# Performance work log

Hardware: AMD Instinct MI355X
Metric: run time of the kernel (lower is better)

Reference implementation:

```python
import jax, jax.numpy as jnp
import numpy as np

HID = 2048
HEADS = 16
HD = HID // HEADS  # 128
EPS = 1e-6


def setup_inputs() -> dict:
    key = jax.random.key(0)
    ks = jax.random.split(key, 9)
    s = 1.0 / np.sqrt(HID)
    return {
        "hidden_states": jax.random.normal(ks[0], (4, 4096, HID), jnp.float32),
        "q_w": jax.random.normal(ks[1], (HID, HID), jnp.float32) * s,
        "q_b": jnp.zeros((HID,), jnp.float32),
        "k_w": jax.random.normal(ks[2], (HID, HID), jnp.float32) * s,
        "k_b": jnp.zeros((HID,), jnp.float32),
        "v_w": jax.random.normal(ks[3], (HID, HID), jnp.float32) * s,
        "v_b": jnp.zeros((HID,), jnp.float32),
        "o_w": jax.random.normal(ks[4], (HID, HID), jnp.float32) * s,
        "o_b": jnp.zeros((HID,), jnp.float32),
    }


def _heads(x, b, s):
    # [B,S,HID] -> [B,H,S,Dh]
    return x.reshape(b, s, HEADS, HD).transpose(0, 2, 1, 3)


def reference(hidden_states, q_w, q_b, k_w, k_b, v_w, v_b, o_w, o_b):
    b, s, _ = hidden_states.shape
    # torch Linear: y = x @ W.T + b
    q = _heads(hidden_states @ q_w.T + q_b, b, s)
    k = _heads(hidden_states @ k_w.T + k_b, b, s)
    v = _heads(hidden_states @ v_w.T + v_b, b, s)
    # kernel feature map: elu(x) + 1
    qp = jax.nn.elu(q) + 1.0
    kp = jax.nn.elu(k) + 1.0
    # KV outer-product reduction over sequence: [B,H,Dh,Dh]
    kv = jnp.einsum('bhsd,bhse->bhde', kp, v)
    # normalizer z = q' @ sum_s k'  -> [B,H,S,1]
    z = jnp.einsum('bhsd,bhd->bhs', qp, kp.sum(axis=2))[..., None]
    attn = jnp.einsum('bhsd,bhde->bhse', qp, kv) / (z + EPS)
    out = attn.transpose(0, 2, 1, 3).reshape(b, s, HID)
    return out @ o_w.T + o_b
```

## Files before the change

### kernel.cpp

```cpp
#include <hip/hip_runtime.h>
#include <hip/hip_bf16.h>

#define HIDC 2048
#define NHEADS 16
#define HDIM 128
#define NB 4
#define NS 4096
#define NROWS (NB*NS)
#define QSTR 6144
#define EPSV 1e-6f

typedef __attribute__((ext_vector_type(8))) short s16x8;
typedef __attribute__((ext_vector_type(4))) float f32x4;
typedef __attribute__((ext_vector_type(8))) unsigned short u16x8;

static __device__ __forceinline__ unsigned short f2b(float f) {
  unsigned int u = __float_as_uint(f);
  u += 0x7fffu + ((u >> 16) & 1u);
  return (unsigned short)(u >> 16);
}
static __device__ __forceinline__ float b2f(unsigned short h) {
  return __uint_as_float(((unsigned int)h) << 16);
}

static __device__ __forceinline__ void gload_lds16(const unsigned short* g, unsigned short* l) {
  __builtin_amdgcn_global_load_lds(
      (const __attribute__((address_space(1))) void*)g,
      (__attribute__((address_space(3))) void*)l, 16, 0, 0);
}

__global__ __launch_bounds__(256) void convert_all(
    const float* __restrict__ hs, const float* __restrict__ qw,
    const float* __restrict__ kw, const float* __restrict__ vw,
    const float* __restrict__ ow,
    unsigned short* __restrict__ hsb, unsigned short* __restrict__ qwb,
    unsigned short* __restrict__ kwb, unsigned short* __restrict__ vwb,
    unsigned short* __restrict__ owb)
{
  int bid = blockIdx.x;
  const float* src; unsigned short* dst; size_t base;
  if (bid < 16384) { src = hs; dst = hsb; base = (size_t)bid << 11; }
  else {
    int t = bid - 16384; int wsel = t >> 11; int wb = t & 2047;
    src = wsel == 0 ? qw : wsel == 1 ? kw : wsel == 2 ? vw : ow;
    dst = wsel == 0 ? qwb : wsel == 1 ? kwb : wsel == 2 ? vwb : owb;
    base = (size_t)wb << 11;
  }
  size_t i = base + ((size_t)threadIdx.x << 3);
  float4 a = *(const float4*)(src + i);
  float4 b = *(const float4*)(src + i + 4);
  u16x8 o;
  o[0] = f2b(a.x); o[1] = f2b(a.y); o[2] = f2b(a.z); o[3] = f2b(a.w);
  o[4] = f2b(b.x); o[5] = f2b(b.y); o[6] = f2b(b.z); o[7] = f2b(b.w);
  *(u16x8*)(dst + i) = o;
}

template<int QKV, int OUT_BF16>
__global__ __launch_bounds__(512, 1) void gemm256(
    const unsigned short* __restrict__ A,
    const unsigned short* __restrict__ B0,
    const unsigned short* __restrict__ B1,
    const unsigned short* __restrict__ B2,
    const float* __restrict__ bias0,
    const float* __restrict__ bias1,
    const float* __restrict__ bias2,
    void* __restrict__ Cp,
    int ntile, int astr, int ostr)
{
  __shared__ unsigned short lds[65536];
  const int tid = threadIdx.x;
  const int lane = tid & 63, wid = tid >> 6;
  const int wr = wid >> 2, wc = wid & 3;
  const int l15 = lane & 15, l4 = lane >> 4;

  const int cpx = (int)gridDim.x >> 3;
  const int bidx = (int)blockIdx.x;
  const int wg = (bidx & 7) * cpx + (bidx >> 3);
  const int csz = ntile << 2;
  const int chunk = wg / csz;
  const int tt = wg % csz;
  const int bm = ((chunk << 2) + (tt & 3)) << 8;
  const int bn = (tt >> 2) << 8;

  const unsigned short* Bp = B0;
  const float* bias = bias0;
  bool act = false;
  int bnw = bn;
  if (QKV) {
    int seg = bn >> 11;
    Bp = seg == 0 ? B0 : (seg == 1 ? B1 : B2);
    bias = seg == 0 ? bias0 : (seg == 1 ? bias1 : bias2);
    act = seg < 2;
    bnw = bn & 2047;
  }

  const int r0 = tid >> 2;
  const int s0 = tid & 3;
  const int scol = ((s0 ^ ((r0 >> 1) & 3)) << 3);
  const unsigned short* ApA  = A  + (size_t)(bm  + r0) * astr + scol;
  const unsigned short* ApA2 = ApA + (size_t)128 * astr;
  const unsigned short* BpB  = Bp + (size_t)(bnw + r0) * HIDC + scol;
  const unsigned short* BpB2 = BpB + (size_t)128 * HIDC;

  const int xa = ((l4 ^ ((l15 >> 1) & 3)) << 3);
  const int abase = ((wr << 7) + l15) * 32 + xa;
  const int bbase = 16384 + ((wc << 6) + l15) * 32 + xa;

  f32x4 acc[8][4] = {};
  s16x8 af[8], bf2[4];

#define LD(off_) (*(const s16x8*)&lds[off_])
#define ST_A(kk_, kt_) { \
    gload_lds16(ApA  + (kt_) + ((kk_) << 5), &lds[wb + ((kk_) << 13) + (tid << 3)]); \
    gload_lds16(ApA2 + (kt_) + ((kk_) << 5), &lds[wb + ((kk_) << 13) + 4096 + (tid << 3)]); }
#define ST_B(kk_, kt_) { \
    gload_lds16(BpB  + (kt_) + ((kk_) << 5), &lds[wb + 16384 + ((kk_) << 13) + (tid << 3)]); \
    gload_lds16(BpB2 + (kt_) + ((kk_) << 5), &lds[wb + 16384 + ((kk_) << 13) + 4096 + (tid << 3)]); }
#define MM16(i0_, i1_, i2_, i3_) { \
    acc[i0_][0] = __builtin_amdgcn_mfma_f32_16x16x32_bf16(af[i0_], bf2[0], acc[i0_][0], 0, 0, 0); \
    acc[i0_][1] = __builtin_amdgcn_mfma_f32_16x16x32_bf16(af[i0_], bf2[1], acc[i0_][1], 0, 0, 0); \
    acc[i0_][2] = __builtin_amdgcn_mfma_f32_16x16x32_bf16(af[i0_], bf2[2], acc[i0_][2], 0, 0, 0); \
    acc[i0_][3] = __builtin_amdgcn_mfma_f32_16x16x32_bf16(af[i0_], bf2[3], acc[i0_][3], 0, 0, 0); \
    acc[i1_][0] = __builtin_amdgcn_mfma_f32_16x16x32_bf16(af[i1_], bf2[0], acc[i1_][0], 0, 0, 0); \
    acc[i1_][1] = __builtin_amdgcn_mfma_f32_16x16x32_bf16(af[i1_], bf2[1], acc[i1_][1], 0, 0, 0); \
    acc[i1_][2] = __builtin_amdgcn_mfma_f32_16x16x32_bf16(af[i1_], bf2[2], acc[i1_][2], 0, 0, 0); \
    acc[i1_][3] = __builtin_amdgcn_mfma_f32_16x16x32_bf16(af[i1_], bf2[3], acc[i1_][3], 0, 0, 0); \
    acc[i2_][0] = __builtin_amdgcn_mfma_f32_16x16x32_bf16(af[i2_], bf2[0], acc[i2_][0], 0, 0, 0); \
    acc[i2_][1] = __builtin_amdgcn_mfma_f32_16x16x32_bf16(af[i2_], bf2[1], acc[i2_][1], 0, 0, 0); \
    acc[i2_][2] = __builtin_amdgcn_mfma_f32_16x16x32_bf16(af[i2_], bf2[2], acc[i2_][2], 0, 0, 0); \
    acc[i2_][3] = __builtin_amdgcn_mfma_f32_16x16x32_bf16(af[i2_], bf2[3], acc[i2_][3], 0, 0, 0); \
    acc[i3_][0] = __builtin_amdgcn_mfma_f32_16x16x32_bf16(af[i3_], bf2[0], acc[i3_][0], 0, 0, 0); \
    acc[i3_][1] = __builtin_amdgcn_mfma_f32_16x16x32_bf16(af[i3_], bf2[1], acc[i3_][1], 0, 0, 0); \
    acc[i3_][2] = __builtin_amdgcn_mfma_f32_16x16x32_bf16(af[i3_], bf2[2], acc[i3_][2], 0, 0, 0); \
    acc[i3_][3] = __builtin_amdgcn_mfma_f32_16x16x32_bf16(af[i3_], bf2[3], acc[i3_][3], 0, 0, 0); }
#define SB   __builtin_amdgcn_sched_barrier(0);
#define BAR  __builtin_amdgcn_s_barrier();
#define LGKM0 asm volatile("s_waitcnt lgkmcnt(0)" ::: "memory");
#define PRON __builtin_amdgcn_s_setprio(1);
#define PROFF __builtin_amdgcn_s_setprio(0);
#define GATE(G_) { if ((G_) == 4) { asm volatile("s_waitcnt vmcnt(4)" ::: "memory"); } \
                   else if ((G_) == 0) { asm volatile("s_waitcnt vmcnt(0)" ::: "memory"); } }

#define DO_TILE(t_, STG, G1, G3) { \
    const int rb = ((t_) & 1) << 15; \
    const int wb = rb ^ 32768; (void)wb; \
    const int kts = ((t_) + 1) << 6; (void)kts; \
     \
    bf2[0] = LD(rb + bbase);        bf2[1] = LD(rb + bbase + 512); \
    bf2[2] = LD(rb + bbase + 1024); bf2[3] = LD(rb + bbase + 1536); \
    af[0] = LD(rb + abase);         af[1] = LD(rb + abase + 512); \
    af[2] = LD(rb + abase + 1024);  af[3] = LD(rb + abase + 1536); \
    if (STG) ST_A(0, kts); \
    SB BAR LGKM0 PRON MM16(0, 1, 2, 3) PROFF BAR \
     \
    af[4] = LD(rb + abase + 2048);  af[5] = LD(rb + abase + 2560); \
    af[6] = LD(rb + abase + 3072);  af[7] = LD(rb + abase + 3584); \
    if (STG) ST_B(0, kts); \
    SB BAR LGKM0 PRON MM16(4, 5, 6, 7) PROFF GATE(G1) BAR \
     \
    bf2[0] = LD(rb + 8192 + bbase);        bf2[1] = LD(rb + 8192 + bbase + 512); \
    bf2[2] = LD(rb + 8192 + bbase + 1024); bf2[3] = LD(rb + 8192 + bbase + 1536); \
    af[0] = LD(rb + 8192 + abase);         af[1] = LD(rb + 8192 + abase + 512); \
    af[2] = LD(rb + 8192 + abase + 1024);  af[3] = LD(rb + 8192 + abase + 1536); \
    if (STG) ST_A(1, kts); \
    SB BAR LGKM0 PRON MM16(0, 1, 2, 3) PROFF BAR \
     \
    af[4] = LD(rb + 8192 + abase + 2048);  af[5] = LD(rb + 8192 + abase + 2560); \
    af[6] = LD(rb + 8192 + abase + 3072);  af[7] = LD(rb + 8192 + abase + 3584); \
    if (STG) ST_B(1, kts); \
    SB BAR LGKM0 PRON MM16(4, 5, 6, 7) PROFF GATE(G3) BAR \
  }

  {
    const int wb = 0;
    ST_A(0, 0); ST_B(0, 0); ST_A(1, 0); ST_B(1, 0);
  }
  asm volatile("s_waitcnt vmcnt(4)" ::: "memory");
  __builtin_amdgcn_s_barrier();

  for (int t = 0; t < 31; ++t) DO_TILE(t, 1, 4, 4)
  DO_TILE(31, 0, 0, -1)

#undef DO_TILE
#undef GATE
#undef PROFF
#undef PRON
#undef LGKM0
#undef BAR
#undef SB
#undef MM16
#undef ST_B
#undef ST_A
#undef LD

  #pragma unroll
  for (int nf = 0; nf < 4; ++nf) {
    const int colw = (wc << 6) + (nf << 4) + l15;
    const float bv = bias[bnw + colw];
    #pragma unroll
    for (int mf = 0; mf < 8; ++mf) {
      #pragma unroll
      for (int r = 0; r < 4; ++r) {
        const int row = bm + (wr << 7) + (mf << 4) + (l4 << 2) + r;
        float v = acc[mf][nf][r] + bv;
        if (QKV) { if (act) v = (v > 0.f) ? (v + 1.f) : __expf(v); }
        const size_t off = (size_t)row * ostr + bn + colw;
        if (OUT_BF16) ((unsigned short*)Cp)[off] = f2b(v);
        else          ((float*)Cp)[off] = v;
      }
    }
  }
}

__global__ __launch_bounds__(256) void kv_partial(
    const unsigned short* __restrict__ kp, const unsigned short* __restrict__ vv,
    float* __restrict__ kvp, float* __restrict__ ksp)
{
  const int bh = blockIdx.x >> 4;
  const int chunk = blockIdx.x & 15;
  const int b = bh >> 4, h = bh & 15;
  const int tid = threadIdx.x;
  const int td = tid >> 4, te = tid & 15;

  __shared__ float kpl[32][128];
  __shared__ float vl[32][132];

  float acc[8][8] = {};
  float ks[8] = {};

  const size_t rowbase = (size_t)b * NS * QSTR + (size_t)h * HDIM;
  const int s0 = chunk * 256;

  for (int st = 0; st < 256; st += 32) {
    __syncthreads();
    #pragma unroll
    for (int i = 0; i < 2; ++i) {
      int idx = tid + (i << 8);
      int row = idx >> 4, q = idx & 15;
      size_t g = rowbase + (size_t)(s0 + st + row) * QSTR + (q << 3);
      u16x8 k8 = *(const u16x8*)(kp + g);
      u16x8 v8 = *(const u16x8*)(vv + g);
      float tk[8], tv[8];
      #pragma unroll
      for (int j = 0; j < 8; ++j) { tk[j] = b2f(k8[j]); tv[j] = b2f(v8[j]); }
      *(float4*)&kpl[row][(q << 3)]     = make_float4(tk[0], tk[1], tk[2], tk[3]);
      *(float4*)&kpl[row][(q << 3) + 4] = make_float4(tk[4], tk[5], tk[6], tk[7]);
      *(float4*)&vl[row][(q << 3)]      = make_float4(tv[0], tv[1], tv[2], tv[3]);
      *(float4*)&vl[row][(q << 3) + 4]  = make_float4(tv[4], tv[5], tv[6], tv[7]);
    }
    __syncthreads();
    #pragma unroll 4
    for (int s = 0; s < 32; ++s) {
      float kd[8], ve[8];
      *(float4*)&kd[0] = *(const float4*)&kpl[s][td << 3];
      *(float4*)&kd[4] = *(const float4*)&kpl[s][(td << 3) + 4];
      *(float4*)&ve[0] = *(const float4*)&vl[s][te << 3];
      *(float4*)&ve[4] = *(const float4*)&vl[s][(te << 3) + 4];
      if (te == 0) {
        #pragma unroll
        for (int i = 0; i < 8; ++i) ks[i] += kd[i];
      }
      #pragma unroll
      for (int i = 0; i < 8; ++i)
        #pragma unroll
        for (int j = 0; j < 8; ++j)
          acc[i][j] += kd[i] * ve[j];
    }
  }

  float* outp = kvp + ((size_t)(chunk * 64 + bh) << 14);
  #pragma unroll
  for (int j = 0; j < 8; ++j) {
    int e = (te << 3) + j;
    float r0[8];
    #pragma unroll
    for (int i = 0; i < 8; ++i) r0[i] = acc[i][j];
    *(float4*)&outp[(size_t)e * HDIM + (td << 3)]     = *(float4*)&r0[0];
    *(float4*)&outp[(size_t)e * HDIM + (td << 3) + 4] = *(float4*)&r0[4];
  }
  if (te == 0) {
    float* kso = ksp + ((size_t)(chunk * 64 + bh) << 7) + (td << 3);
    #pragma unroll
    for (int i = 0; i < 8; ++i) kso[i] = ks[i];
  }
}

__global__ __launch_bounds__(256) void kv_reduce(
    const float* __restrict__ kvp, float* __restrict__ kvT)
{
  int i = blockIdx.x * 256 + threadIdx.x;
  float s = 0.f;
  #pragma unroll
  for (int c = 0; c < 16; ++c) s += kvp[(size_t)c * (64 * 16384) + i];
  kvT[i] = s;
}

__global__ __launch_bounds__(256) void attn_ker(
    const unsigned short* __restrict__ qp, const float* __restrict__ kvT,
    const float* __restrict__ ksp, unsigned short* __restrict__ attn)
{
  const int bh = blockIdx.x >> 5, stile = blockIdx.x & 31;
  const int b = bh >> 4, h = bh & 15;
  const int tid = threadIdx.x;
  const int lane = tid & 63, w = tid >> 6;
  const int l15 = lane & 15, l4 = lane >> 4;

  __shared__ unsigned short Qs[128][136];
  __shared__ unsigned short Ks[128][136];
  __shared__ float ksl[128];
  __shared__ float zs[128];

  const size_t qbase = ((size_t)b * NS + (size_t)stile * 128) * QSTR + (size_t)h * HDIM;

  #pragma unroll
  for (int i = 0; i < 8; ++i) {
    int idx = tid + (i << 8);
    int row = idx >> 4, q = idx & 15;
    u16x8 v8 = *(const u16x8*)(qp + qbase + (size_t)row * QSTR + (q << 3));
    *(u16x8*)&Qs[row][q << 3] = v8;
  }
  const float* kvb = kvT + ((size_t)bh << 14);
  #pragma unroll
  for (int i = 0; i < 16; ++i) {
    int idx = tid + (i << 8);
    int row = idx >> 5, q = idx & 31;
    float4 v4 = *(const float4*)(kvb + (size_t)row * HDIM + (q << 2));
    ushort4 w4; w4.x = f2b(v4.x); w4.y = f2b(v4.y); w4.z = f2b(v4.z); w4.w = f2b(v4.w);
    *(ushort4*)&Ks[row][q << 2] = w4;
  }
  if (tid < 128) {
    float s = 0.f;
    #pragma unroll
    for (int c = 0; c < 16; ++c) s += ksp[((size_t)(c * 64 + bh) << 7) + tid];
    ksl[tid] = s;
  }
  __syncthreads();
  if (tid < 128) {
    float z = 0.f;
    #pragma unroll
    for (int dq = 0; dq < 16; ++dq) {
      u16x8 qv = *(const u16x8*)&Qs[tid][dq << 3];
      #pragma unroll
      for (int j = 0; j < 8; ++j) z += b2f(qv[j]) * ksl[(dq << 3) + j];
    }
    zs[tid] = 1.f / (z + EPSV);
  }
  __syncthreads();

  f32x4 acc[2][8] = {};
  #pragma unroll
  for (int kk = 0; kk < 4; ++kk) {
    s16x8 a[2], bb[8];
    #pragma unroll
    for (int mf = 0; mf < 2; ++mf)
      a[mf] = *(const s16x8*)&Qs[(w << 5) + (mf << 4) + l15][(kk << 5) + (l4 << 3)];
    #pragma unroll
    for (int nf = 0; nf < 8; ++nf)
      bb[nf] = *(const s16x8*)&Ks[(nf << 4) + l15][(kk << 5) + (l4 << 3)];
    #pragma unroll
    for (int mf = 0; mf < 2; ++mf)
      #pragma unroll
      for (int nf = 0; nf < 8; ++nf)
        acc[mf][nf] = __builtin_amdgcn_mfma_f32_16x16x32_bf16(a[mf], bb[nf], acc[mf][nf], 0, 0, 0);
  }

  #pragma unroll
  for (int mf = 0; mf < 2; ++mf) {
    #pragma unroll
    for (int r = 0; r < 4; ++r) {
      const int rl = (w << 5) + (mf << 4) + (l4 << 2) + r;
      const float zi = zs[rl];
      #pragma unroll
      for (int nf = 0; nf < 8; ++nf) {
        const int e = (nf << 4) + l15;
        attn[qbase + (size_t)rl * QSTR + e] = f2b(acc[mf][nf][r] * zi);
      }
    }
  }
}

extern "C" void kernel_launch(void* const* d_in, const int* in_sizes, int n_in,
                              void* d_out, int out_size, void* d_ws, size_t ws_size,
                              hipStream_t stream) {
  const float* hs = (const float*)d_in[0];
  const float* qw = (const float*)d_in[1];
  const float* qb = (const float*)d_in[2];
  const float* kw = (const float*)d_in[3];
  const float* kb = (const float*)d_in[4];
  const float* vw = (const float*)d_in[5];
  const float* vb = (const float*)d_in[6];
  const float* ow = (const float*)d_in[7];
  const float* ob = (const float*)d_in[8];

  char* w = (char*)d_ws;
  unsigned short* hsb = (unsigned short*)(w);
  unsigned short* qwb = (unsigned short*)(w + 67108864);
  unsigned short* kwb = (unsigned short*)(w + 75497472);
  unsigned short* vwb = (unsigned short*)(w + 83886080);
  unsigned short* owb = (unsigned short*)(w + 92274688);
  unsigned short* qkv = (unsigned short*)(w + 100663296);
  float* kvp = (float*)(w);
  float* ksp = (float*)(w + 67108864);
  float* kvT = (float*)(w + 67108864 + 524288);

  convert_all<<<dim3(24576), dim3(256), 0, stream>>>(hs, qw, kw, vw, ow, hsb, qwb, kwb, vwb, owb);
  gemm256<1, 1><<<dim3(1536), dim3(512), 0, stream>>>(
      hsb, qwb, kwb, vwb, qb, kb, vb, qkv, 24, HIDC, QSTR);
  kv_partial<<<dim3(1024), dim3(256), 0, stream>>>(qkv + 2048, qkv + 4096, kvp, ksp);
  kv_reduce<<<dim3(4096), dim3(256), 0, stream>>>(kvp, kvT);
  attn_ker<<<dim3(2048), dim3(256), 0, stream>>>(qkv, kvT, ksp, qkv + 4096);
  gemm256<0, 0><<<dim3(512), dim3(512), 0, stream>>>(
      qkv + 4096, owb, owb, owb, ob, ob, ob, d_out, 8, QSTR, HIDC);
}
```

Baseline: 784.5 us.

## Switch GEMM inner loop to 32x32x16 MFMA with reworked LDS swizzle and phases

Replaces the 16x16x32 bf16 MFMA tiling with 32x32x16 instructions, so each wave keeps 4x2 32x32 accumulator tiles instead of 8x4 16x16 tiles. The LDS XOR swizzle and the fragment addressing are redone to match the 32-lane fragment layout. The pipeline is restructured into per-k-half phases, with one barrier per phase and A and B staging issued together, replacing the four sub-phases and their double barriers. The aim is fewer LDS reads and fewer MFMA issues for the same work, plus lower synchronization overhead. In exchange, overlap between loads and compute may be weaker.

After: 771.4 us. Within noise of the previous version (-1.7%).

```diff
diff --git a/kernel.cpp b/kernel.cpp
--- a/kernel.cpp
+++ b/kernel.cpp
@@ -12,6 +12,7 @@
 
 typedef __attribute__((ext_vector_type(8))) short s16x8;
 typedef __attribute__((ext_vector_type(4))) float f32x4;
+typedef __attribute__((ext_vector_type(16))) float f32x16;
 typedef __attribute__((ext_vector_type(8))) unsigned short u16x8;
 
 static __device__ __forceinline__ unsigned short f2b(float f) {
@@ -71,7 +72,7 @@
   const int tid = threadIdx.x;
   const int lane = tid & 63, wid = tid >> 6;
   const int wr = wid >> 2, wc = wid & 3;
-  const int l15 = lane & 15, l4 = lane >> 4;
+  const int l31 = lane & 31, l5 = lane >> 5;
 
   const int cpx = (int)gridDim.x >> 3;
   const int bidx = (int)blockIdx.x;
@@ -96,18 +97,20 @@
 
   const int r0 = tid >> 2;
   const int s0 = tid & 3;
-  const int scol = ((s0 ^ ((r0 >> 1) & 3)) << 3);
+  const int scol = ((s0 ^ ((r0 >> 3) & 3)) << 3);
   const unsigned short* ApA  = A  + (size_t)(bm  + r0) * astr + scol;
   const unsigned short* ApA2 = ApA + (size_t)128 * astr;
   const unsigned short* BpB  = Bp + (size_t)(bnw + r0) * HIDC + scol;
   const unsigned short* BpB2 = BpB + (size_t)128 * HIDC;
 
-  const int xa = ((l4 ^ ((l15 >> 1) & 3)) << 3);
-  const int abase = ((wr << 7) + l15) * 32 + xa;
-  const int bbase = 16384 + ((wc << 6) + l15) * 32 + xa;
-
-  f32x4 acc[8][4] = {};
-  s16x8 af[8], bf2[4];
+  const int xr = (l31 >> 3) & 3;
+  const int sj0 = ((l5 ^ xr) << 3);
+  const int sj1 = (((2 + l5) ^ xr) << 3);
+  const int abase = ((wr << 7) + l31) * 32;
+  const int bbase = 16384 + ((wc << 6) + l31) * 32;
+
+  f32x16 acc[4][2] = {};
+  s16x8 a[4][2], b[2][2];
 
 #define LD(off_) (*(const s16x8*)&lds[off_])
 #define ST_A(kk_, kt_) { \
@@ -116,93 +119,75 @@
 #define ST_B(kk_, kt_) { \
     gload_lds16(BpB  + (kt_) + ((kk_) << 5), &lds[wb + 16384 + ((kk_) << 13) + (tid << 3)]); \
     gload_lds16(BpB2 + (kt_) + ((kk_) << 5), &lds[wb + 16384 + ((kk_) << 13) + 4096 + (tid << 3)]); }
-#define MM16(i0_, i1_, i2_, i3_) { \
-    acc[i0_][0] = __builtin_amdgcn_mfma_f32_16x16x32_bf16(af[i0_], bf2[0], acc[i0_][0], 0, 0, 0); \
-    acc[i0_][1] = __builtin_amdgcn_mfma_f32_16x16x32_bf16(af[i0_], bf2[1], acc[i0_][1], 0, 0, 0); \
-    acc[i0_][2] = __builtin_amdgcn_mfma_f32_16x16x32_bf16(af[i0_], bf2[2], acc[i0_][2], 0, 0, 0); \
-    acc[i0_][3] = __builtin_amdgcn_mfma_f32_16x16x32_bf16(af[i0_], bf2[3], acc[i0_][3], 0, 0, 0); \
-    acc[i1_][0] = __builtin_amdgcn_mfma_f32_16x16x32_bf16(af[i1_], bf2[0], acc[i1_][0], 0, 0, 0); \
-    acc[i1_][1] = __builtin_amdgcn_mfma_f32_16x16x32_bf16(af[i1_], bf2[1], acc[i1_][1], 0, 0, 0); \
-    acc[i1_][2] = __builtin_amdgcn_mfma_f32_16x16x32_bf16(af[i1_], bf2[2], acc[i1_][2], 0, 0, 0); \
-    acc[i1_][3] = __builtin_amdgcn_mfma_f32_16x16x32_bf16(af[i1_], bf2[3], acc[i1_][3], 0, 0, 0); \
-    acc[i2_][0] = __builtin_amdgcn_mfma_f32_16x16x32_bf16(af[i2_], bf2[0], acc[i2_][0], 0, 0, 0); \
-    acc[i2_][1] = __builtin_amdgcn_mfma_f32_16x16x32_bf16(af[i2_], bf2[1], acc[i2_][1], 0, 0, 0); \
-    acc[i2_][2] = __builtin_amdgcn_mfma_f32_16x16x32_bf16(af[i2_], bf2[2], acc[i2_][2], 0, 0, 0); \
-    acc[i2_][3] = __builtin_amdgcn_mfma_f32_16x16x32_bf16(af[i2_], bf2[3], acc[i2_][3], 0, 0, 0); \
-    acc[i3_][0] = __builtin_amdgcn_mfma_f32_16x16x32_bf16(af[i3_], bf2[0], acc[i3_][0], 0, 0, 0); \
-    acc[i3_][1] = __builtin_amdgcn_mfma_f32_16x16x32_bf16(af[i3_], bf2[1], acc[i3_][1], 0, 0, 0); \
-    acc[i3_][2] = __builtin_amdgcn_mfma_f32_16x16x32_bf16(af[i3_], bf2[2], acc[i3_][2], 0, 0, 0); \
-    acc[i3_][3] = __builtin_amdgcn_mfma_f32_16x16x32_bf16(af[i3_], bf2[3], acc[i3_][3], 0, 0, 0); }
+#define MM8(j_) { \
+    acc[0][0] = __builtin_amdgcn_mfma_f32_32x32x16_bf16(a[0][j_], b[0][j_], acc[0][0], 0, 0, 0); \
+    acc[0][1] = __builtin_amdgcn_mfma_f32_32x32x16_bf16(a[0][j_], b[1][j_], acc[0][1], 0, 0, 0); \
+    acc[1][0] = __builtin_amdgcn_mfma_f32_32x32x16_bf16(a[1][j_], b[0][j_], acc[1][0], 0, 0, 0); \
+    acc[1][1] = __builtin_amdgcn_mfma_f32_32x32x16_bf16(a[1][j_], b[1][j_], acc[1][1], 0, 0, 0); \
+    acc[2][0] = __builtin_amdgcn_mfma_f32_32x32x16_bf16(a[2][j_], b[0][j_], acc[2][0], 0, 0, 0); \
+    acc[2][1] = __builtin_amdgcn_mfma_f32_32x32x16_bf16(a[2][j_], b[1][j_], acc[2][1], 0, 0, 0); \
+    acc[3][0] = __builtin_amdgcn_mfma_f32_32x32x16_bf16(a[3][j_], b[0][j_], acc[3][0], 0, 0, 0); \
+    acc[3][1] = __builtin_amdgcn_mfma_f32_32x32x16_bf16(a[3][j_], b[1][j_], acc[3][1], 0, 0, 0); }
 #define SB   __builtin_amdgcn_sched_barrier(0);
 #define BAR  __builtin_amdgcn_s_barrier();
-#define LGKM0 asm volatile("s_waitcnt lgkmcnt(0)" ::: "memory");
 #define PRON __builtin_amdgcn_s_setprio(1);
 #define PROFF __builtin_amdgcn_s_setprio(0);
-#define GATE(G_) { if ((G_) == 4) { asm volatile("s_waitcnt vmcnt(4)" ::: "memory"); } \
-                   else if ((G_) == 0) { asm volatile("s_waitcnt vmcnt(0)" ::: "memory"); } }
-
-#define DO_TILE(t_, STG, G1, G3) { \
-    const int rb = ((t_) & 1) << 15; \
-    const int wb = rb ^ 32768; (void)wb; \
-    const int kts = ((t_) + 1) << 6; (void)kts; \
-     \
-    bf2[0] = LD(rb + bbase);        bf2[1] = LD(rb + bbase + 512); \
-    bf2[2] = LD(rb + bbase + 1024); bf2[3] = LD(rb + bbase + 1536); \
-    af[0] = LD(rb + abase);         af[1] = LD(rb + abase + 512); \
-    af[2] = LD(rb + abase + 1024);  af[3] = LD(rb + abase + 1536); \
-    if (STG) ST_A(0, kts); \
-    SB BAR LGKM0 PRON MM16(0, 1, 2, 3) PROFF BAR \
-     \
-    af[4] = LD(rb + abase + 2048);  af[5] = LD(rb + abase + 2560); \
-    af[6] = LD(rb + abase + 3072);  af[7] = LD(rb + abase + 3584); \
-    if (STG) ST_B(0, kts); \
-    SB BAR LGKM0 PRON MM16(4, 5, 6, 7) PROFF GATE(G1) BAR \
-     \
-    bf2[0] = LD(rb + 8192 + bbase);        bf2[1] = LD(rb + 8192 + bbase + 512); \
-    bf2[2] = LD(rb + 8192 + bbase + 1024); bf2[3] = LD(rb + 8192 + bbase + 1536); \
-    af[0] = LD(rb + 8192 + abase);         af[1] = LD(rb + 8192 + abase + 512); \
-    af[2] = LD(rb + 8192 + abase + 1024);  af[3] = LD(rb + 8192 + abase + 1536); \
-    if (STG) ST_A(1, kts); \
-    SB BAR LGKM0 PRON MM16(0, 1, 2, 3) PROFF BAR \
-     \
-    af[4] = LD(rb + 8192 + abase + 2048);  af[5] = LD(rb + 8192 + abase + 2560); \
-    af[6] = LD(rb + 8192 + abase + 3072);  af[7] = LD(rb + 8192 + abase + 3584); \
-    if (STG) ST_B(1, kts); \
-    SB BAR LGKM0 PRON MM16(4, 5, 6, 7) PROFF GATE(G3) BAR \
+
+#define PHASE(rb_, kk_, GATE, STG, kts_) { \
+    if ((GATE) == 4)      { asm volatile("s_waitcnt vmcnt(4)" ::: "memory"); } \
+    else if ((GATE) == 0) { asm volatile("s_waitcnt vmcnt(0)" ::: "memory"); } \
+    BAR \
+    const int pb = (rb_) + ((kk_) << 13); \
+    b[0][0] = LD(pb + bbase + sj0);        b[0][1] = LD(pb + bbase + sj1); \
+    b[1][0] = LD(pb + bbase + 1024 + sj0); b[1][1] = LD(pb + bbase + 1024 + sj1); \
+    a[0][0] = LD(pb + abase + sj0);        a[0][1] = LD(pb + abase + sj1); \
+    a[1][0] = LD(pb + abase + 1024 + sj0); a[1][1] = LD(pb + abase + 1024 + sj1); \
+    a[2][0] = LD(pb + abase + 2048 + sj0); a[2][1] = LD(pb + abase + 2048 + sj1); \
+    a[3][0] = LD(pb + abase + 3072 + sj0); a[3][1] = LD(pb + abase + 3072 + sj1); \
+    if (STG) { ST_A(kk_, kts_); ST_B(kk_, kts_); } \
+    SB PRON MM8(0) MM8(1) PROFF \
   }
 
   {
     const int wb = 0;
-    ST_A(0, 0); ST_B(0, 0); ST_A(1, 0); ST_B(1, 0);
-  }
-  asm volatile("s_waitcnt vmcnt(4)" ::: "memory");
-  __builtin_amdgcn_s_barrier();
-
-  for (int t = 0; t < 31; ++t) DO_TILE(t, 1, 4, 4)
-  DO_TILE(31, 0, 0, -1)
-
-#undef DO_TILE
-#undef GATE
+    ST_A(0, 0); ST_B(0, 0);
+    ST_A(1, 0); ST_B(1, 0);
+  }
+
+  for (int t = 0; t < 31; ++t) {
+    const int rb = (t & 1) << 15;
+    const int wb = rb ^ 32768;
+    const int kts = (t + 1) << 6;
+    PHASE(rb, 0, 4, 1, kts)
+    PHASE(rb, 1, 4, 1, kts)
+  }
+  {
+    const int rb = (31 & 1) << 15;
+    const int wb = 0; (void)wb;
+    PHASE(rb, 0, 4, 0, 0)
+    PHASE(rb, 1, 0, 0, 0)
+  }
+
+#undef PHASE
 #undef PROFF
 #undef PRON
-#undef LGKM0
 #undef BAR
 #undef SB
-#undef MM16
+#undef MM8
 #undef ST_B
 #undef ST_A
 #undef LD
 
   #pragma unroll
-  for (int nf = 0; nf < 4; ++nf) {
-    const int colw = (wc << 6) + (nf << 4) + l15;
-    const float bv = bias[bnw + colw];
-    #pragma unroll
-    for (int mf = 0; mf < 8; ++mf) {
-      #pragma unroll
-      for (int r = 0; r < 4; ++r) {
-        const int row = bm + (wr << 7) + (mf << 4) + (l4 << 2) + r;
-        float v = acc[mf][nf][r] + bv;
+  for (int mf = 0; mf < 4; ++mf) {
+    #pragma unroll
+    for (int nf = 0; nf < 2; ++nf) {
+      const int colw = (wc << 6) + (nf << 5) + l31;
+      const float bv = bias[bnw + colw];
+      #pragma unroll
+      for (int reg = 0; reg < 16; ++reg) {
+        const int row = bm + (wr << 7) + (mf << 5) + (reg & 3) + ((reg >> 2) << 3) + (l5 << 2);
+        float v = acc[mf][nf][reg] + bv;
         if (QKV) { if (act) v = (v > 0.f) ? (v + 1.f) : __expf(v); }
         const size_t off = (size_t)row * ostr + bn + colw;
         if (OUT_BF16) ((unsigned short*)Cp)[off] = f2b(v);
```
